# Kernel optimization log

Hardware: AMD Instinct MI355X
Metric: run time of the kernel (lower is better)

The kernel has to match this reference:

```python
import jax, jax.numpy as jnp
import numpy as np

H = 32; W = 32; C = 128; K = 3
FS = K * K                      # filter_size = 9
CH = H - K + 1; CW = W - K + 1
F = CH * CW                     # num_convs = 900
HW = H * W                      # 1024
TEMP = 1.0                      # softmax_temp
EPS = 1e-5                      # masked_softmax epsilon
B = 8


def _build_masks():
    # local_indices[f] = flat indices of the K x K window f (row-major),
    # matching compute_input_mask with stride=1, no stochastic stride.
    idx = np.zeros((F, FS), dtype=np.int32)
    f = 0
    for i in range(CH):
        for j in range(CW):
            rows = np.arange(i, i + K)[:, None]
            cols = np.arange(j, j + K)[None, :]
            idx[f] = (rows * W + cols).reshape(-1)
            f += 1
    # global mask = (1 - local_mask) * (1 - padding_mask); padding_mask == 0 for 'valid'
    gmask = np.ones((F, HW), dtype=np.float32)
    gmask[np.arange(F)[:, None], idx] = 0.0
    return jnp.asarray(idx), jnp.asarray(gmask)


def setup_inputs() -> dict:
    key = jax.random.key(0)
    ks = jax.random.split(key, 8)
    bound = 1.0 / np.sqrt(C)  # torch nn.Linear default init
    u = lambda k, shape: jax.random.uniform(k, shape, jnp.float32, -bound, bound)
    batch = jax.random.normal(ks[0], (B, H, W, C), jnp.float32)
    Wq = u(ks[1], (C, C)); bq = u(ks[2], (C,))
    Wk = u(ks[3], (C, C)); bk = u(ks[4], (C,))
    wv = u(ks[5], (C, 1)); bv = u(ks[6], (1,))
    local_indices, gmask = _build_masks()
    return {"batch": batch, "Wq": Wq, "bq": bq, "Wk": Wk, "bk": bk,
            "wv": wv, "bv": bv, "gmask": gmask, "local_indices": local_indices}


def reference(batch, Wq, bq, Wk, bk, wv, bv, gmask, local_indices):
    # Approach '4': per-window local queries attend over global (non-window)
    # pixels; scalar values gate the local patch pixels; gated patch sums to
    # one output pixel per window. Valid padding => local pixels are unmasked
    # and the masked softmax zeroes out window/padding positions, so the
    # per-window masked linear transforms reduce exactly to full-image
    # transforms gathered/masked afterwards (no [F,B,H,W,C] materialization).
    b = batch.shape[0]
    xf = batch.reshape(b, HW, C)
    Q = xf @ Wq.T + bq                         # [B,HW,C] query_transform
    Kf = xf @ Wk.T + bk                        # [B,HW,C] key_transform
    V = (xf @ wv + bv)[..., 0]                 # [B,HW]   value_transform (C->1)
    Qg = Q[:, local_indices]                   # [B,F,FS,C] local queries (gather)
    Xl = xf[:, local_indices]                  # [B,F,FS,C] local patch features
    compat = jnp.einsum('bfpc,bqc->bfpq', Qg, Kf) / TEMP   # [B,F,FS,HW]
    # masked_softmax: exp * mask / (sum + eps), no max-subtraction (faithful)
    exps = jnp.exp(compat) * gmask[None, :, None, :]
    attn = exps / (exps.sum(-1, keepdims=True) + EPS)
    gates = jnp.einsum('bfpq,bq->bfp', attn, V)            # [B,F,FS] scalar gates
    out = jnp.einsum('bfp,bfpc->bfc', gates, Xl)           # [B,F,C]
    return out.reshape(b, CH, CW, C)
```

## Files before the change

kernel.cpp:

```cpp
#include <hip/hip_runtime.h>

#define BATCH 8
#define HW_N  1024
#define CD    128
#define W_IMG 32
#define CH_O  30
#define F_N   900

#define OFF_Q16 0u
#define OFF_K16 2097152u
#define OFF_V   4194304u
#define OFF_D   4227072u
#define OFF_TP  5046272u
#define OFF_TVP 5570560u
#define OFF_WQH 6094848u
#define OFF_WQL 6127616u
#define OFF_WKH 6160384u
#define OFF_WKL 6193152u

typedef _Float16 f16x8 __attribute__((ext_vector_type(8)));
typedef _Float16 f16x4 __attribute__((ext_vector_type(4)));
typedef float    f32x4 __attribute__((ext_vector_type(4)));

__device__ __forceinline__ size_t frag_off(int R, int k) {
    return (size_t)(R >> 4) * 2048 +
           (size_t)((((k >> 5) * 4 + ((k >> 3) & 3)) * 128) + ((R & 15) * 8) + (k & 7));
}

__device__ __forceinline__ void async16(const void* g, void* l) {
    __builtin_amdgcn_global_load_lds(
        (const __attribute__((address_space(1))) unsigned int*)g,
        (__attribute__((address_space(3))) unsigned int*)l,
        16, 0, 0);
}

__global__ __launch_bounds__(256) void prep_kernel(
    const float* __restrict__ Wq, const float* __restrict__ Wk,
    _Float16* __restrict__ WqH, _Float16* __restrict__ WqL,
    _Float16* __restrict__ WkH, _Float16* __restrict__ WkL)
{
    int id = blockIdx.x * 256 + threadIdx.x;
    int c  = id >> 4;
    int kc = id & 15;
    size_t src = (size_t)c * CD + kc * 8;
    size_t dst = frag_off(c, kc * 8);

    float vq[8], vk[8];
    *(float4*)&vq[0] = *(const float4*)&Wq[src];
    *(float4*)&vq[4] = *(const float4*)&Wq[src + 4];
    *(float4*)&vk[0] = *(const float4*)&Wk[src];
    *(float4*)&vk[4] = *(const float4*)&Wk[src + 4];

    f16x8 qh, ql, kh, kl;
#pragma unroll
    for (int e = 0; e < 8; ++e) {
        _Float16 h = (_Float16)vq[e];
        qh[e] = h; ql[e] = (_Float16)(vq[e] - (float)h);
        _Float16 h2 = (_Float16)vk[e];
        kh[e] = h2; kl[e] = (_Float16)(vk[e] - (float)h2);
    }
    *(f16x8*)&WqH[dst] = qh;
    *(f16x8*)&WqL[dst] = ql;
    *(f16x8*)&WkH[dst] = kh;
    *(f16x8*)&WkL[dst] = kl;
}

__global__ __launch_bounds__(256) void qkv_kernel(
    const float* __restrict__ xf,
    const float* __restrict__ bq, const float* __restrict__ bk,
    const float* __restrict__ wv, const float* __restrict__ bv,
    const _Float16* __restrict__ WqH, const _Float16* __restrict__ WqL,
    const _Float16* __restrict__ WkH, const _Float16* __restrict__ WkL,
    _Float16* __restrict__ Q16, _Float16* __restrict__ K16,
    float* __restrict__ V)
{
    __shared__ float    xs[16][132];
    __shared__ _Float16 xh[2048];
    __shared__ _Float16 xl[2048];

    const int t = threadIdx.x;
    const int rowbase = blockIdx.x * 16;

#pragma unroll
    for (int m = 0; m < 2; ++m) {
        int id = t + 256 * m;
        int r  = id >> 5;
        int c4 = id & 31;
        float4 v4 = *(const float4*)&xf[(size_t)(rowbase + r) * CD + c4 * 4];
        *(float4*)&xs[r][c4 * 4] = v4;
        int c = c4 * 4;
        int off = ((c >> 5) * 4 + ((c >> 3) & 3)) * 128 + r * 8 + (c & 7);
        float vv[4] = {v4.x, v4.y, v4.z, v4.w};
        f16x4 hh, ll;
#pragma unroll
        for (int e = 0; e < 4; ++e) {
            _Float16 h = (_Float16)vv[e];
            hh[e] = h; ll[e] = (_Float16)(vv[e] - (float)h);
        }
        *(f16x4*)&xh[off] = hh;
        *(f16x4*)&xl[off] = ll;
    }
    __syncthreads();

    const int w    = t >> 6;
    const int lane = t & 63;
    const int q    = lane >> 4;
    const int i    = lane & 15;

    f32x4 aq[2], ak[2];
#pragma unroll
    for (int ct = 0; ct < 2; ++ct) {
        aq[ct] = (f32x4){0.f, 0.f, 0.f, 0.f};
        ak[ct] = (f32x4){0.f, 0.f, 0.f, 0.f};
    }

#pragma unroll
    for (int ks = 0; ks < 4; ++ks) {
        const int aoff = (ks * 4 + q) * 128 + i * 8;
        f16x8 ah = *(f16x8*)&xh[aoff];
        f16x8 al = *(f16x8*)&xl[aoff];
#pragma unroll
        for (int ct = 0; ct < 2; ++ct) {
            size_t boff = (size_t)(w * 2 + ct) * 2048 + (size_t)(ks * 4 + q) * 128 + i * 8;
            f16x8 bqh = *(const f16x8*)&WqH[boff];
            f16x8 bql = *(const f16x8*)&WqL[boff];
            f16x8 bkh = *(const f16x8*)&WkH[boff];
            f16x8 bkl = *(const f16x8*)&WkL[boff];
            aq[ct] = __builtin_amdgcn_mfma_f32_16x16x32_f16(ah, bqh, aq[ct], 0, 0, 0);
            aq[ct] = __builtin_amdgcn_mfma_f32_16x16x32_f16(ah, bql, aq[ct], 0, 0, 0);
            aq[ct] = __builtin_amdgcn_mfma_f32_16x16x32_f16(al, bqh, aq[ct], 0, 0, 0);
            ak[ct] = __builtin_amdgcn_mfma_f32_16x16x32_f16(ah, bkh, ak[ct], 0, 0, 0);
            ak[ct] = __builtin_amdgcn_mfma_f32_16x16x32_f16(ah, bkl, ak[ct], 0, 0, 0);
            ak[ct] = __builtin_amdgcn_mfma_f32_16x16x32_f16(al, bkh, ak[ct], 0, 0, 0);
        }
    }

#pragma unroll
    for (int ct = 0; ct < 2; ++ct) {
        int c = (w * 2 + ct) * 16 + i;
        float bqv = bq[c], bkv = bk[c];
#pragma unroll
        for (int g = 0; g < 4; ++g) {
            int R = rowbase + q * 4 + g;
            size_t o = frag_off(R, c);
            Q16[o] = (_Float16)(aq[ct][g] + bqv);
            K16[o] = (_Float16)(ak[ct][g] + bkv);
        }
    }

    if (t < 16) {
        float s = 0.f;
#pragma unroll 8
        for (int k = 0; k < CD; ++k) s += xs[t][k] * wv[k];
        V[rowbase + t] = s + bv[0];
    }
}

#define A_OFF 0
#define B_OFF 16384
#define VS_OFF 32768
#define SCR2 16896
#define ATTN_LDS_TOTAL 33792

__global__ __launch_bounds__(256) void attn_kernel(
    const _Float16* __restrict__ Q16, const _Float16* __restrict__ K16,
    const float* __restrict__ V,
    double* __restrict__ Tp, double* __restrict__ TVp,
    float* __restrict__ D)
{
    extern __shared__ char lds[];
    _Float16* Ah = (_Float16*)(lds + A_OFF);
    _Float16* Bh = (_Float16*)(lds + B_OFF);
    float*    Vs = (float*)(lds + VS_OFF);

    const int b  = blockIdx.x;
    const int rb = blockIdx.y;
    const int cb = blockIdx.z;
    const int t  = threadIdx.x;
    const int w    = t >> 6;
    const int lane = t & 63;
    const int q    = lane >> 4;
    const int i    = lane & 15;
    const int wy = w >> 1, wx = w & 1;

    if (t < 128) Vs[t] = V[b * HW_N + cb * 128 + t];

    f32x4 acc[4][4];
#pragma unroll
    for (int r = 0; r < 4; ++r)
#pragma unroll
        for (int f = 0; f < 4; ++f) acc[r][f] = (f32x4){0.f, 0.f, 0.f, 0.f};

    const size_t abase = (size_t)(b * 8 + rb) * 16384;
    const size_t bbase = (size_t)(b * 8 + cb) * 16384;

    for (int kh = 0; kh < 2; ++kh) {
        __syncthreads();
#pragma unroll
        for (int m = 0; m < 4; ++m) {
            int id = t + 256 * m;
            size_t goff = (size_t)(id >> 7) * 2048 + kh * 1024 + (id & 127) * 8;
            int loff = id * 8;
            async16(Q16 + abase + goff, Ah + loff);
            async16(K16 + bbase + goff, Bh + loff);
        }
        asm volatile("s_waitcnt vmcnt(0)" ::: "memory");
        __syncthreads();

#pragma unroll
        for (int kcl = 0; kcl < 2; ++kcl) {
            f16x8 a4[4], b4[4];
#pragma unroll
            for (int r = 0; r < 4; ++r) {
                int ao = (((wy * 4 + r) * 2 + kcl) * 4 + q) * 128 + i * 8;
                a4[r] = *(f16x8*)&Ah[ao];
                int bo = (((wx * 4 + r) * 2 + kcl) * 4 + q) * 128 + i * 8;
                b4[r] = *(f16x8*)&Bh[bo];
            }
#pragma unroll
            for (int r = 0; r < 4; ++r)
#pragma unroll
                for (int f = 0; f < 4; ++f)
                    acc[r][f] = __builtin_amdgcn_mfma_f32_16x16x32_f16(
                        a4[r], b4[f], acc[r][f], 0, 0, 0);
        }
    }

    float st[4][4], stv[4][4];
#pragma unroll
    for (int r = 0; r < 4; ++r)
#pragma unroll
        for (int g = 0; g < 4; ++g) { st[r][g] = 0.f; stv[r][g] = 0.f; }

    const bool band = (cb - rb <= 1) && (rb - cb <= 1);

#pragma unroll
    for (int f = 0; f < 4; ++f) {
        int col_local = wx * 64 + f * 16 + i;
        int hw_c = cb * 128 + col_local;
        float v = Vs[col_local];
        int cimg_r = hw_c >> 5, cimg_c = hw_c & 31;
#pragma unroll
        for (int r = 0; r < 4; ++r)
#pragma unroll
            for (int g = 0; g < 4; ++g) {
                float e = __expf(acc[r][f][g]);
                st[r][g]  += e;
                stv[r][g] += e * v;
                if (band) {
                    int row_local = wy * 64 + r * 16 + q * 4 + g;
                    int hw_r = rb * 128 + row_local;
                    int dy = cimg_r - (hw_r >> 5);
                    int dx = cimg_c - (hw_r & 31);
                    if ((unsigned)(dy + 2) <= 4u && (unsigned)(dx + 2) <= 4u)
                        D[(size_t)(b * HW_N + hw_r) * 25 + (dy + 2) * 5 + (dx + 2)] = e;
                }
            }
    }

    __syncthreads();
    float* scrT  = (float*)lds;
    float* scrTV = (float*)(lds + SCR2);
#pragma unroll
    for (int r = 0; r < 4; ++r)
#pragma unroll
        for (int g = 0; g < 4; ++g) {
            int rl = wy * 64 + r * 16 + q * 4 + g;
            scrT [rl * 33 + wx * 16 + i] = st[r][g];
            scrTV[rl * 33 + wx * 16 + i] = stv[r][g];
        }
    __syncthreads();
    if (t < 128) {
        double s = 0.0;
#pragma unroll
        for (int c = 0; c < 32; ++c) s += (double)scrT[t * 33 + c];
        Tp[(size_t)(b * HW_N + rb * 128 + t) * 8 + cb] = s;
    } else {
        int tt = t - 128;
        double s = 0.0;
#pragma unroll
        for (int c = 0; c < 32; ++c) s += (double)scrTV[tt * 33 + c];
        TVp[(size_t)(b * HW_N + rb * 128 + tt) * 8 + cb] = s;
    }
}

__global__ __launch_bounds__(256) void gate_out_kernel(
    const float* __restrict__ xf, const float* __restrict__ V,
    const double* __restrict__ Tp, const double* __restrict__ TVp,
    const float* __restrict__ D, float* __restrict__ out)
{
    const int fi = blockIdx.x;
    const int b  = blockIdx.y;
    const int t  = threadIdx.x;

    __shared__ float  xs[96 * 128];
    __shared__ float  gates[30][9];
    __shared__ double Ts[96], TVs[96];

#pragma unroll
    for (int m = 0; m < 12; ++m) {
        int id   = t + 256 * m;
        int srow = id >> 5;
        int c4   = id & 31;
        int r3   = srow >> 5, colc = srow & 31;
        *(float4*)&xs[srow * 128 + c4 * 4] =
            *(const float4*)&xf[((size_t)(b * 32 + fi + r3) * 32 + colc) * CD + c4 * 4];
    }

    if (t < 96) {
        int R = b * HW_N + (fi + (t >> 5)) * W_IMG + (t & 31);
        double s = 0.0;
#pragma unroll
        for (int c = 0; c < 8; ++c) s += Tp[(size_t)R * 8 + c];
        Ts[t] = s;
    } else if (t >= 128 && t < 224) {
        int tt = t - 128;
        int R = b * HW_N + (fi + (tt >> 5)) * W_IMG + (tt & 31);
        double s = 0.0;
#pragma unroll
        for (int c = 0; c < 8; ++c) s += TVp[(size_t)R * 8 + c];
        TVs[tt] = s;
    }
    __syncthreads();

    for (int g = t; g < 270; g += 256) {
        int fj = g / 9, p = g % 9;
        int pr = p / 3, pc = p % 3;
        int lrow = pr * 32 + fj + pc;
        int ip = (fi + pr) * W_IMG + (fj + pc);
        const float* Drow = &D[(size_t)(b * HW_N + ip) * 25];
        double se = 0.0, sev = 0.0;
#pragma unroll
        for (int qq = 0; qq < 9; ++qq) {
            int qr = qq / 3, qc = qq % 3;
            float e = Drow[(qr - pr + 2) * 5 + (qc - pc + 2)];
            se  += (double)e;
            sev += (double)(e * V[b * HW_N + (fi + qr) * W_IMG + (fj + qc)]);
        }
        double denom = Ts[lrow] - se + 1e-5;
        double numer = TVs[lrow] - sev;
        gates[fj][p] = (float)(numer / denom);
    }
    __syncthreads();

    const int c   = t & 127;
    const int fjg = t >> 7;
#pragma unroll
    for (int it = 0; it < 15; ++it) {
        int fj = fjg * 15 + it;
        float o = 0.f;
#pragma unroll
        for (int p = 0; p < 9; ++p) {
            int pr = p / 3, pc = p % 3;
            o += gates[fj][p] * xs[(pr * 32 + fj + pc) * 128 + c];
        }
        out[((size_t)(b * F_N) + fi * CH_O + fj) * CD + c] = o;
    }
}

extern "C" void kernel_launch(void* const* d_in, const int* in_sizes, int n_in,
                              void* d_out, int out_size, void* d_ws, size_t ws_size,
                              hipStream_t stream)
{
    (void)in_sizes; (void)n_in; (void)out_size; (void)ws_size;
    const float* batch = (const float*)d_in[0];
    const float* Wq    = (const float*)d_in[1];
    const float* bq    = (const float*)d_in[2];
    const float* Wk    = (const float*)d_in[3];
    const float* bk    = (const float*)d_in[4];
    const float* wv    = (const float*)d_in[5];
    const float* bv    = (const float*)d_in[6];

    char*      ws  = (char*)d_ws;
    _Float16*  Q16 = (_Float16*)(ws + OFF_Q16);
    _Float16*  K16 = (_Float16*)(ws + OFF_K16);
    float*     V   = (float*)(ws + OFF_V);
    float*     D   = (float*)(ws + OFF_D);
    double*    Tp  = (double*)(ws + OFF_TP);
    double*    TVp = (double*)(ws + OFF_TVP);
    _Float16*  WqH = (_Float16*)(ws + OFF_WQH);
    _Float16*  WqL = (_Float16*)(ws + OFF_WQL);
    _Float16*  WkH = (_Float16*)(ws + OFF_WKH);
    _Float16*  WkL = (_Float16*)(ws + OFF_WKL);
    float*     out = (float*)d_out;

    prep_kernel<<<dim3(8), dim3(256), 0, stream>>>(Wq, Wk, WqH, WqL, WkH, WkL);
    qkv_kernel<<<dim3(512), dim3(256), 0, stream>>>(batch, bq, bk, wv, bv,
                                                    WqH, WqL, WkH, WkL,
                                                    Q16, K16, V);
    attn_kernel<<<dim3(8, 8, 8), dim3(256), ATTN_LDS_TOTAL, stream>>>(
        Q16, K16, V, Tp, TVp, D);
    gate_out_kernel<<<dim3(CH_O, BATCH), dim3(256), 0, stream>>>(batch, V, Tp, TVp, D, out);
}
```

Before: 98.45 us.

## Drop split-fp16 QK projection and weight prep kernel; vectorize gate output

```diff
diff --git a/kernel.cpp b/kernel.cpp
--- a/kernel.cpp
+++ b/kernel.cpp
@@ -13,10 +13,6 @@
 #define OFF_D   4227072u
 #define OFF_TP  5046272u
 #define OFF_TVP 5570560u
-#define OFF_WQH 6094848u
-#define OFF_WQL 6127616u
-#define OFF_WKH 6160384u
-#define OFF_WKL 6193152u
 
 typedef _Float16 f16x8 __attribute__((ext_vector_type(8)));
 typedef _Float16 f16x4 __attribute__((ext_vector_type(4)));
@@ -34,49 +30,16 @@
         16, 0, 0);
 }
 
-__global__ __launch_bounds__(256) void prep_kernel(
-    const float* __restrict__ Wq, const float* __restrict__ Wk,
-    _Float16* __restrict__ WqH, _Float16* __restrict__ WqL,
-    _Float16* __restrict__ WkH, _Float16* __restrict__ WkL)
-{
-    int id = blockIdx.x * 256 + threadIdx.x;
-    int c  = id >> 4;
-    int kc = id & 15;
-    size_t src = (size_t)c * CD + kc * 8;
-    size_t dst = frag_off(c, kc * 8);
-
-    float vq[8], vk[8];
-    *(float4*)&vq[0] = *(const float4*)&Wq[src];
-    *(float4*)&vq[4] = *(const float4*)&Wq[src + 4];
-    *(float4*)&vk[0] = *(const float4*)&Wk[src];
-    *(float4*)&vk[4] = *(const float4*)&Wk[src + 4];
-
-    f16x8 qh, ql, kh, kl;
-#pragma unroll
-    for (int e = 0; e < 8; ++e) {
-        _Float16 h = (_Float16)vq[e];
-        qh[e] = h; ql[e] = (_Float16)(vq[e] - (float)h);
-        _Float16 h2 = (_Float16)vk[e];
-        kh[e] = h2; kl[e] = (_Float16)(vk[e] - (float)h2);
-    }
-    *(f16x8*)&WqH[dst] = qh;
-    *(f16x8*)&WqL[dst] = ql;
-    *(f16x8*)&WkH[dst] = kh;
-    *(f16x8*)&WkL[dst] = kl;
-}
-
 __global__ __launch_bounds__(256) void qkv_kernel(
     const float* __restrict__ xf,
-    const float* __restrict__ bq, const float* __restrict__ bk,
+    const float* __restrict__ Wq, const float* __restrict__ bq,
+    const float* __restrict__ Wk, const float* __restrict__ bk,
     const float* __restrict__ wv, const float* __restrict__ bv,
-    const _Float16* __restrict__ WqH, const _Float16* __restrict__ WqL,
-    const _Float16* __restrict__ WkH, const _Float16* __restrict__ WkL,
     _Float16* __restrict__ Q16, _Float16* __restrict__ K16,
     float* __restrict__ V)
 {
     __shared__ float    xs[16][132];
     __shared__ _Float16 xh[2048];
-    __shared__ _Float16 xl[2048];
 
     const int t = threadIdx.x;
     const int rowbase = blockIdx.x * 16;
@@ -90,15 +53,10 @@
         *(float4*)&xs[r][c4 * 4] = v4;
         int c = c4 * 4;
         int off = ((c >> 5) * 4 + ((c >> 3) & 3)) * 128 + r * 8 + (c & 7);
-        float vv[4] = {v4.x, v4.y, v4.z, v4.w};
-        f16x4 hh, ll;
-#pragma unroll
-        for (int e = 0; e < 4; ++e) {
-            _Float16 h = (_Float16)vv[e];
-            hh[e] = h; ll[e] = (_Float16)(vv[e] - (float)h);
-        }
+        f16x4 hh;
+        hh[0] = (_Float16)v4.x; hh[1] = (_Float16)v4.y;
+        hh[2] = (_Float16)v4.z; hh[3] = (_Float16)v4.w;
         *(f16x4*)&xh[off] = hh;
-        *(f16x4*)&xl[off] = ll;
     }
     __syncthreads();
 
@@ -118,20 +76,25 @@
     for (int ks = 0; ks < 4; ++ks) {
         const int aoff = (ks * 4 + q) * 128 + i * 8;
         f16x8 ah = *(f16x8*)&xh[aoff];
-        f16x8 al = *(f16x8*)&xl[aoff];
 #pragma unroll
         for (int ct = 0; ct < 2; ++ct) {
-            size_t boff = (size_t)(w * 2 + ct) * 2048 + (size_t)(ks * 4 + q) * 128 + i * 8;
-            f16x8 bqh = *(const f16x8*)&WqH[boff];
-            f16x8 bql = *(const f16x8*)&WqL[boff];
-            f16x8 bkh = *(const f16x8*)&WkH[boff];
-            f16x8 bkl = *(const f16x8*)&WkL[boff];
-            aq[ct] = __builtin_amdgcn_mfma_f32_16x16x32_f16(ah, bqh, aq[ct], 0, 0, 0);
-            aq[ct] = __builtin_amdgcn_mfma_f32_16x16x32_f16(ah, bql, aq[ct], 0, 0, 0);
-            aq[ct] = __builtin_amdgcn_mfma_f32_16x16x32_f16(al, bqh, aq[ct], 0, 0, 0);
-            ak[ct] = __builtin_amdgcn_mfma_f32_16x16x32_f16(ah, bkh, ak[ct], 0, 0, 0);
-            ak[ct] = __builtin_amdgcn_mfma_f32_16x16x32_f16(ah, bkl, ak[ct], 0, 0, 0);
-            ak[ct] = __builtin_amdgcn_mfma_f32_16x16x32_f16(al, bkh, ak[ct], 0, 0, 0);
+            const int c = (w * 2 + ct) * 16 + i;
+            const size_t wo = (size_t)c * CD + ks * 32 + q * 8;
+            float4 wq0 = *(const float4*)&Wq[wo];
+            float4 wq1 = *(const float4*)&Wq[wo + 4];
+            float4 wk0 = *(const float4*)&Wk[wo];
+            float4 wk1 = *(const float4*)&Wk[wo + 4];
+            f16x8 bq8, bk8;
+            bq8[0] = (_Float16)wq0.x; bq8[1] = (_Float16)wq0.y;
+            bq8[2] = (_Float16)wq0.z; bq8[3] = (_Float16)wq0.w;
+            bq8[4] = (_Float16)wq1.x; bq8[5] = (_Float16)wq1.y;
+            bq8[6] = (_Float16)wq1.z; bq8[7] = (_Float16)wq1.w;
+            bk8[0] = (_Float16)wk0.x; bk8[1] = (_Float16)wk0.y;
+            bk8[2] = (_Float16)wk0.z; bk8[3] = (_Float16)wk0.w;
+            bk8[4] = (_Float16)wk1.x; bk8[5] = (_Float16)wk1.y;
+            bk8[6] = (_Float16)wk1.z; bk8[7] = (_Float16)wk1.w;
+            aq[ct] = __builtin_amdgcn_mfma_f32_16x16x32_f16(ah, bq8, aq[ct], 0, 0, 0);
+            ak[ct] = __builtin_amdgcn_mfma_f32_16x16x32_f16(ah, bk8, ak[ct], 0, 0, 0);
         }
     }
 
@@ -294,7 +257,7 @@
     const int t  = threadIdx.x;
 
     __shared__ float  xs[96 * 128];
-    __shared__ float  gates[30][9];
+    __shared__ float  gates[32][9];
     __shared__ double Ts[96], TVs[96];
 
 #pragma unroll
@@ -343,18 +306,22 @@
     }
     __syncthreads();
 
-    const int c   = t & 127;
-    const int fjg = t >> 7;
-#pragma unroll
-    for (int it = 0; it < 15; ++it) {
-        int fj = fjg * 15 + it;
-        float o = 0.f;
-#pragma unroll
-        for (int p = 0; p < 9; ++p) {
-            int pr = p / 3, pc = p % 3;
-            o += gates[fj][p] * xs[(pr * 32 + fj + pc) * 128 + c];
-        }
-        out[((size_t)(b * F_N) + fi * CH_O + fj) * CD + c] = o;
+    const int c4  = t & 31;
+    const int fjl = t >> 5;
+#pragma unroll
+    for (int it = 0; it < 4; ++it) {
+        int fj = fjl + 8 * it;
+        if (fj < CH_O) {
+            f32x4 o = (f32x4){0.f, 0.f, 0.f, 0.f};
+#pragma unroll
+            for (int p = 0; p < 9; ++p) {
+                int pr = p / 3, pc = p % 3;
+                f32x4 x = *(f32x4*)&xs[(pr * 32 + fj + pc) * 128 + c4 * 4];
+                float gv = gates[fj][p];
+                o += gv * x;
+            }
+            *(f32x4*)&out[((size_t)(b * F_N) + fi * CH_O + fj) * CD + c4 * 4] = o;
+        }
     }
 }
 
@@ -378,15 +345,9 @@
     float*     D   = (float*)(ws + OFF_D);
     double*    Tp  = (double*)(ws + OFF_TP);
     double*    TVp = (double*)(ws + OFF_TVP);
-    _Float16*  WqH = (_Float16*)(ws + OFF_WQH);
-    _Float16*  WqL = (_Float16*)(ws + OFF_WQL);
-    _Float16*  WkH = (_Float16*)(ws + OFF_WKH);
-    _Float16*  WkL = (_Float16*)(ws + OFF_WKL);
     float*     out = (float*)d_out;
 
-    prep_kernel<<<dim3(8), dim3(256), 0, stream>>>(Wq, Wk, WqH, WqL, WkH, WkL);
-    qkv_kernel<<<dim3(512), dim3(256), 0, stream>>>(batch, bq, bk, wv, bv,
-                                                    WqH, WqL, WkH, WkL,
+    qkv_kernel<<<dim3(512), dim3(256), 0, stream>>>(batch, Wq, bq, Wk, bk, wv, bv,
                                                     Q16, K16, V);
     attn_kernel<<<dim3(8, 8, 8), dim3(256), ATTN_LDS_TOTAL, stream>>>(
         Q16, K16, V, Tp, TVp, D);
```

New measurement: 101.9 us. 1.03x slower.
